# Performance work log

Hardware: AMD Instinct MI355X
Metric: run time of the kernel (lower is better)

The kernel has to match this reference:

```python
import jax, jax.numpy as jnp
import numpy as np

C, Q, F, N = 50000, 8, 256, 65536  # num_classes, instances/class, feat_len, n_proposals


def setup_inputs() -> dict:
    key = jax.random.key(0)
    kf, kl = jax.random.split(key)
    return {
        "features": jax.random.normal(kf, (N, F), jnp.float32),
        "queue": jnp.zeros((C, Q, F), jnp.float32),
        "pid_labels": jax.random.randint(kl, (N,), 0, C, jnp.int32),
        "tail": jnp.zeros((C,), jnp.int32),
    }


def _update(features, queue, pid_labels, tail):
    # Parallel-equivalent of the sequential per-label circular-buffer write:
    # proposal i with label l writes to slot (tail[l] + occ_i) % Q where occ_i is
    n = features.shape[0]
    c, q, f = queue.shape
    valid = (pid_labels >= 0) & (pid_labels < c)
    lab = jnp.where(valid, pid_labels, c)  # sentinel c for invalid labels
    order = jnp.argsort(lab)  # stable sort groups equal labels, preserves order
    sl = lab[order]
    first = jnp.searchsorted(sl, sl, side="left").astype(lab.dtype)
    occ_sorted = jnp.arange(n, dtype=lab.dtype) - first  # occurrence index within label group
    occ = jnp.zeros(n, lab.dtype).at[order].set(occ_sorted)
    lab_c = jnp.clip(lab, 0, c - 1)
    slot = (tail[lab_c].astype(lab.dtype) + occ) % q
    flat = jnp.where(valid, lab_c * q + slot, 0)  # flat (class, slot) bucket
    writer = jnp.where(valid, jnp.arange(n, dtype=jnp.int32), -1)
    last = jax.ops.segment_max(writer, flat, num_segments=c * q)  # last proposal hitting each bucket
    written = last >= 0
    qf = jnp.where(written[:, None], features[jnp.clip(last, 0)], queue.reshape(c * q, f))
    return qf.reshape(c, q, f)


def reference(features, queue, pid_labels, tail):
    return _update(features, queue, pid_labels, tail)
```

## Files before the change

### kernel.cpp

```cpp
#include <hip/hip_runtime.h>


#define HBLK 1024

__global__ void k_hist(const int* __restrict__ lab, int* __restrict__ cnt,
                       int N, int C) {
    int b = blockIdx.x;
    int i = b * HBLK + threadIdx.x;
    if (i < N) {
        int l = lab[i];
        if (l >= 0 && l < C) atomicAdd(&cnt[(size_t)b * C + l], 1);
    }
}

__global__ void k_prefix(int* __restrict__ cnt, int* __restrict__ ktot,
                         int C, int NB) {
    int l = blockIdx.x * blockDim.x + threadIdx.x;
    if (l >= C) return;
    int run = 0;
    for (int b = 0; b < NB; ++b) {
        int t = cnt[(size_t)b * C + l];
        cnt[(size_t)b * C + l] = run;
        run += t;
    }
    ktot[l] = run;
}

__global__ void k_slots(const int* __restrict__ lab, const int* __restrict__ tail,
                        const int* __restrict__ cnt, const int* __restrict__ ktot,
                        int* __restrict__ idx, int N, int C, int Q) {
    __shared__ int slab[HBLK];
    int b = blockIdx.x;
    int t = threadIdx.x;
    int i = b * HBLK + t;
    int l = (i < N) ? lab[i] : -1;
    slab[t] = l;
    __syncthreads();
    if (l < 0 || l >= C) return;
    int local = 0;
    for (int j = 0; j < t; ++j) local += (slab[j] == l) ? 1 : 0;
    int occ = cnt[(size_t)b * C + l] + local;
    int kk = ktot[l];
    if (occ >= kk - Q) {
        int s = (tail[l] + occ) % Q;
        if (s < 0) s += Q;
        idx[l * Q + s] = i;
    }
}

__global__ void k_gather(const float4* __restrict__ feat,
                         const float4* __restrict__ queue,
                         const int* __restrict__ idx,
                         float4* __restrict__ out,
                         long long total4, int F4) {
    long long g = (long long)blockIdx.x * blockDim.x + threadIdx.x;
    if (g >= total4) return;
    int r = (int)(g / F4);
    int c = (int)(g - (long long)r * F4);
    int id = idx[r];
    const float4* src = (id >= 0) ? (feat + (size_t)id * F4 + c)
                                  : (queue + (size_t)r * F4 + c);
    out[g] = *src;
}

extern "C" void kernel_launch(void* const* d_in, const int* in_sizes, int n_in,
                              void* d_out, int out_size, void* d_ws, size_t ws_size,
                              hipStream_t stream) {
    const float* feat  = (const float*)d_in[0];
    const float* queue = (const float*)d_in[1];
    const int*   lab   = (const int*)d_in[2];
    const int*   tail  = (const int*)d_in[3];

    const int N = in_sizes[2];
    const int C = in_sizes[3];
    const int F = in_sizes[0] / N;
    const int Q = in_sizes[1] / (C * F);
    const int NB = (N + HBLK - 1) / HBLK;

    int* idx  = (int*)d_ws;
    int* cnt  = idx + (size_t)C * Q;
    int* ktot = cnt + (size_t)NB * C;

    hipMemsetAsync(idx, 0xFF, (size_t)C * Q * sizeof(int), stream);
    hipMemsetAsync(cnt, 0x00, (size_t)NB * C * sizeof(int), stream);

    k_hist<<<NB, HBLK, 0, stream>>>(lab, cnt, N, C);
    k_prefix<<<(C + 255) / 256, 256, 0, stream>>>(cnt, ktot, C, NB);
    k_slots<<<NB, HBLK, 0, stream>>>(lab, tail, cnt, ktot, idx, N, C, Q);

    const int F4 = F / 4;
    const long long total4 = (long long)C * Q * F4;
    const int gblocks = (int)((total4 + 255) / 256);
    k_gather<<<gblocks, 256, 0, stream>>>((const float4*)feat,
                                          (const float4*)queue, idx,
                                          (float4*)d_out, total4, F4);
}
```

Baseline: 194.5 us.

## Fold workspace memsets into kernels and use grid-stride nontemporal gather

Removes the two hipMemsetAsync calls: the per-block histogram rows are now zeroed inside k_hist, and the idx buffer is set to -1 inside k_prefix. The gather kernel becomes a grid-stride loop capped at 2048 blocks, with a shift/mask fast path when F4==64 and nontemporal loads and stores to avoid cache pollution on the ~400MB output stream. This drops two memset launches and their separate passes over memory, at the cost of per-thread strided idx initialization in k_prefix.

Result: no change. 192.2 us (-1.2%).

```diff
diff --git a/kernel.cpp b/kernel.cpp
--- a/kernel.cpp
+++ b/kernel.cpp
@@ -1,20 +1,26 @@
 #include <hip/hip_runtime.h>
 
+
+typedef float vf4 __attribute__((ext_vector_type(4)));
 
 #define HBLK 1024
 
 __global__ void k_hist(const int* __restrict__ lab, int* __restrict__ cnt,
                        int N, int C) {
     int b = blockIdx.x;
-    int i = b * HBLK + threadIdx.x;
+    int t = threadIdx.x;
+    int* row = cnt + (size_t)b * C;
+    for (int j = t; j < C; j += HBLK) row[j] = 0;
+    __syncthreads();
+    int i = b * HBLK + t;
     if (i < N) {
         int l = lab[i];
-        if (l >= 0 && l < C) atomicAdd(&cnt[(size_t)b * C + l], 1);
+        if (l >= 0 && l < C) atomicAdd(&row[l], 1);
     }
 }
 
 __global__ void k_prefix(int* __restrict__ cnt, int* __restrict__ ktot,
-                         int C, int NB) {
+                         int* __restrict__ idx, int C, int NB, int Q) {
     int l = blockIdx.x * blockDim.x + threadIdx.x;
     if (l >= C) return;
     int run = 0;
@@ -24,6 +30,7 @@
         run += t;
     }
     ktot[l] = run;
+    for (int q = 0; q < Q; ++q) idx[l * Q + q] = -1;
 }
 
 __global__ void k_slots(const int* __restrict__ lab, const int* __restrict__ tail,
@@ -48,19 +55,35 @@
     }
 }
 
-__global__ void k_gather(const float4* __restrict__ feat,
-                         const float4* __restrict__ queue,
+__global__ void k_gather(const vf4* __restrict__ feat,
+                         const vf4* __restrict__ queue,
                          const int* __restrict__ idx,
-                         float4* __restrict__ out,
+                         vf4* __restrict__ out,
                          long long total4, int F4) {
-    long long g = (long long)blockIdx.x * blockDim.x + threadIdx.x;
-    if (g >= total4) return;
-    int r = (int)(g / F4);
-    int c = (int)(g - (long long)r * F4);
-    int id = idx[r];
-    const float4* src = (id >= 0) ? (feat + (size_t)id * F4 + c)
-                                  : (queue + (size_t)r * F4 + c);
-    out[g] = *src;
+    long long stride = (long long)gridDim.x * blockDim.x;
+    if (F4 == 64) {
+        for (long long g = (long long)blockIdx.x * blockDim.x + threadIdx.x;
+             g < total4; g += stride) {
+            int r = (int)(g >> 6);
+            int c = (int)(g & 63);
+            int id = idx[r];
+            const vf4* src = (id >= 0) ? (feat + ((size_t)id << 6) + c)
+                                       : (queue + ((size_t)r << 6) + c);
+            vf4 v = __builtin_nontemporal_load(src);
+            __builtin_nontemporal_store(v, &out[g]);
+        }
+    } else {
+        for (long long g = (long long)blockIdx.x * blockDim.x + threadIdx.x;
+             g < total4; g += stride) {
+            int r = (int)(g / F4);
+            int c = (int)(g - (long long)r * F4);
+            int id = idx[r];
+            const vf4* src = (id >= 0) ? (feat + (size_t)id * F4 + c)
+                                       : (queue + (size_t)r * F4 + c);
+            vf4 v = __builtin_nontemporal_load(src);
+            __builtin_nontemporal_store(v, &out[g]);
+        }
+    }
 }
 
 extern "C" void kernel_launch(void* const* d_in, const int* in_sizes, int n_in,
@@ -81,17 +104,16 @@
     int* cnt  = idx + (size_t)C * Q;
     int* ktot = cnt + (size_t)NB * C;
 
-    hipMemsetAsync(idx, 0xFF, (size_t)C * Q * sizeof(int), stream);
-    hipMemsetAsync(cnt, 0x00, (size_t)NB * C * sizeof(int), stream);
-
     k_hist<<<NB, HBLK, 0, stream>>>(lab, cnt, N, C);
-    k_prefix<<<(C + 255) / 256, 256, 0, stream>>>(cnt, ktot, C, NB);
+    k_prefix<<<(C + 255) / 256, 256, 0, stream>>>(cnt, ktot, idx, C, NB, Q);
     k_slots<<<NB, HBLK, 0, stream>>>(lab, tail, cnt, ktot, idx, N, C, Q);
 
     const int F4 = F / 4;
     const long long total4 = (long long)C * Q * F4;
-    const int gblocks = (int)((total4 + 255) / 256);
-    k_gather<<<gblocks, 256, 0, stream>>>((const float4*)feat,
-                                          (const float4*)queue, idx,
-                                          (float4*)d_out, total4, F4);
+    int gblocks = 2048;
+    long long need = (total4 + 255) / 256;
+    if (need < gblocks) gblocks = (int)need;
+    k_gather<<<gblocks, 256, 0, stream>>>((const vf4*)feat,
+                                          (const vf4*)queue, idx,
+                                          (vf4*)d_out, total4, F4);
 }
```
